# Performance work log

Measured on AMD Instinct MI355X. Metric: run time of the kernel, lower is better.

Reference implementation:

```python
import jax, jax.numpy as jnp
import numpy as np

D_EQUI, D_INV, D_MSG, N_HEADS, D_FF = 64, 256, 64, 8, 256
D_EDGE_IN, D_EDGE_OUT = 64, 64
D_OUT = D_EQUI + N_HEADS + D_EDGE_OUT  # 136
IN_FEATS = 2 * D_MSG + D_EQUI + D_EDGE_IN  # 256
B, N = 4, 256
NEG_INF = -1e9  # finite stand-in for -inf in adj_to_attn_mask


def setup_inputs() -> dict:
    key = jax.random.key(0)
    ks = jax.random.split(key, 20)
    def rn(k, shape, scale):
        return jax.random.normal(k, shape, dtype=jnp.float32) * scale
    inp = {
        "equis": rn(ks[0], (B, N, 3, D_EQUI), 1.0),
        "invs": rn(ks[1], (B, N, D_INV), 1.0),
        "edges": rn(ks[2], (B, N, N, D_EDGE_IN), 1.0),
        "adj_matrix": jax.random.randint(ks[3], (B, N, N), 0, 2, dtype=jnp.int32),
        # _PairwiseMessages params
        "Wq": rn(ks[4], (D_MSG, D_INV), D_INV ** -0.5),
        "bq": jnp.zeros((D_MSG,), jnp.float32),
        "Wk": rn(ks[5], (D_MSG, D_INV), D_INV ** -0.5),
        "bk": jnp.zeros((D_MSG,), jnp.float32),
        "W1": rn(ks[6], (D_FF, IN_FEATS), IN_FEATS ** -0.5),
        "b1": jnp.zeros((D_FF,), jnp.float32),
        "W2": rn(ks[7], (D_OUT, D_FF), D_FF ** -0.5),
        "b2": jnp.zeros((D_OUT,), jnp.float32),
        # _EquiAttention params (no bias)
        "Wc": rn(ks[8], (D_EQUI, D_EQUI), D_EQUI ** -0.5),
        "Wa": rn(ks[9], (D_EQUI, D_EQUI), D_EQUI ** -0.5),
        # _InvAttention params
        "Wi": rn(ks[10], (D_INV, D_INV), D_INV ** -0.5),
        "bi": jnp.zeros((D_INV,), jnp.float32),
        "Wo": rn(ks[11], (D_INV, D_INV), D_INV ** -0.5),
        "bo": jnp.zeros((D_INV,), jnp.float32),
    }
    return inp


def _forward(equis, invs, edges, adj_matrix, Wq, bq, Wk, bk, W1, b1, W2, b2, Wc, Wa, Wi, bi, Wo, bo):
    # ---- _PairwiseMessages ----
    # per-channel dot products over the 3 coordinates: [B, Nq, Nk, d_equi]
    dotprods = jnp.einsum("bqcd,bkcd->bqkd", equis, equis)
    q_msg = invs @ Wq.T + bq          # [B, N, d_msg]
    k_msg = invs @ Wk.T + bk          # [B, N, d_msg]
    Nq = invs.shape[1]
    pairwise = jnp.concatenate(
        (
            jnp.broadcast_to(q_msg[:, :, None, :], (B, Nq, Nq, D_MSG)),
            jnp.broadcast_to(k_msg[:, None, :, :], (B, Nq, Nq, D_MSG)),
            dotprods,
            edges,
        ),
        axis=-1,
    )  # [B, Nq, Nk, in_feats]
    h = jax.nn.silu(pairwise @ W1.T + b1)
    messages = h @ W2.T + b2          # [B, Nq, Nk, d_out]

    equi_msg = messages[..., :D_EQUI]
    inv_msg = messages[..., D_EQUI : D_EQUI + N_HEADS]
    edge_out = messages[..., D_EQUI + N_HEADS :]

    attn_mask = jnp.where(adj_matrix > 0, 0.0, NEG_INF).astype(equi_msg.dtype)  # [B,Nq,Nk]

    # ---- _EquiAttention ----
    attn_e = jax.nn.softmax(equi_msg + attn_mask[..., None], axis=2)  # [B,Nq,Nk,d_equi]
    proj_equi = equis @ Wc.T                                          # [B,Nk,3,d_equi]
    attn_out_e = jnp.einsum("bqkd,bkcd->bqcd", attn_e, proj_equi)     # [B,Nq,3,d_equi]
    w_e = jnp.sqrt(jnp.sum(attn_e ** 2, axis=2))                      # [B,Nq,d_equi]
    attn_out_e = attn_out_e * w_e[:, :, None, :]
    equi_updates = attn_out_e @ Wa.T

    # ---- _InvAttention ----
    attn_i = jax.nn.softmax(inv_msg + attn_mask[..., None], axis=2)   # [B,Nq,Nk,H]
    proj_feats = invs @ Wi.T + bi                                     # [B,Nk,d_inv]
    head_feats = proj_feats.reshape(B, Nq, N_HEADS, D_INV // N_HEADS)
    attn_out_i = jnp.einsum("bqkh,bkhd->bqhd", attn_i, head_feats)    # [B,Nq,H,d_head]
    w_i = jnp.sqrt(jnp.sum(attn_i ** 2, axis=2))                      # [B,Nq,H]
    attn_out_i = attn_out_i * w_i[..., None]
    inv_updates = attn_out_i.reshape(B, Nq, D_INV) @ Wo.T + bo

    return equi_updates, inv_updates, edge_out


def reference(equis, invs, edges, adj_matrix, Wq, bq, Wk, bk, W1, b1, W2, b2, Wc, Wa, Wi, bi, Wo, bo):
    return _forward(equis, invs, edges, adj_matrix, Wq, bq, Wk, bk, W1, b1, W2, b2, Wc, Wa, Wi, bi, Wo, bo)
```

## Files before the change

kernel.cpp:

```cpp
#include <hip/hip_runtime.h>
#include <hip/hip_bf16.h>
#include <cstdint>


typedef __bf16 bf16x4_t __attribute__((ext_vector_type(4)));
typedef __bf16 bf16x8_t __attribute__((ext_vector_type(8)));
typedef float  f32x4_t  __attribute__((ext_vector_type(4)));

#define SP 76
#define KV 32

__device__ __forceinline__ int swzX(int row, int col) {
    return row * 192 + (col ^ ((row & 7) << 3));
}
__device__ __forceinline__ int swzH(int row, int col) {
    return (row << 8) + (col ^ ((row & 7) << 3));
}

__device__ __forceinline__ bf16x8_t cvt8(f32x4_t a, f32x4_t b) {
    bf16x8_t r;
    r[0] = (__bf16)a.x; r[1] = (__bf16)a.y; r[2] = (__bf16)a.z; r[3] = (__bf16)a.w;
    r[4] = (__bf16)b.x; r[5] = (__bf16)b.y; r[6] = (__bf16)b.z; r[7] = (__bf16)b.w;
    return r;
}
__device__ __forceinline__ bf16x4_t cvt4(f32x4_t a) {
    bf16x4_t r;
    r[0] = (__bf16)a.x; r[1] = (__bf16)a.y; r[2] = (__bf16)a.z; r[3] = (__bf16)a.w;
    return r;
}

__global__ __launch_bounds__(256) void semla_pre(
    const float* __restrict__ invs, const float* __restrict__ equis,
    const float* __restrict__ Wq, const float* __restrict__ bq,
    const float* __restrict__ Wk, const float* __restrict__ bk,
    const float* __restrict__ Wc, const float* __restrict__ Wi, const float* __restrict__ bi,
    const float* __restrict__ W1, const float* __restrict__ W2,
    __bf16* __restrict__ W1bf, __bf16* __restrict__ W2bf,
    float* __restrict__ qc, float* __restrict__ kmsg,
    float* __restrict__ pTE, float* __restrict__ pTF)
{
    const int blk = blockIdx.x, tid = threadIdx.x;
    if (blk < 256) {
        const int r0 = blk * 4;
        __shared__ __align__(16) float sInv4[4][256];
        __shared__ __align__(16) float sEqu4[4][192];
        __shared__ __align__(16) float sQm4[4][64];
        #pragma unroll
        for (int j = 0; j < 4; ++j) {
            sInv4[j][tid] = invs[(size_t)(r0 + j) * 256 + tid];
            if (tid < 192) sEqu4[j][tid] = equis[(size_t)(r0 + j) * 192 + tid];
        }
        __syncthreads();
        {
            float acc[4] = {0.f, 0.f, 0.f, 0.f};
            const float* w = &Wi[tid * 256];
            for (int i = 0; i < 256; i += 4) {
                f32x4_t ww = *(const f32x4_t*)&w[i];
                #pragma unroll
                for (int j = 0; j < 4; ++j) {
                    const float* x = &sInv4[j][i];
                    acc[j] += ww.x * x[0] + ww.y * x[1] + ww.z * x[2] + ww.w * x[3];
                }
            }
            const float bb = bi[tid];
            #pragma unroll
            for (int j = 0; j < 4; ++j) {
                const int bb_ = (r0 + j) >> 8, nl = (r0 + j) & 255;
                pTF[((size_t)bb_ * 256 + tid) * 256 + nl] = acc[j] + bb;
            }
        }
        if (tid < 128) {
            const int d = tid & 63;
            const float* w = (tid < 64) ? &Wq[d * 256] : &Wk[d * 256];
            float acc[4] = {0.f, 0.f, 0.f, 0.f};
            for (int i = 0; i < 256; i += 4) {
                f32x4_t ww = *(const f32x4_t*)&w[i];
                #pragma unroll
                for (int j = 0; j < 4; ++j) {
                    const float* x = &sInv4[j][i];
                    acc[j] += ww.x * x[0] + ww.y * x[1] + ww.z * x[2] + ww.w * x[3];
                }
            }
            if (tid < 64) {
                const float bb = bq[d];
                #pragma unroll
                for (int j = 0; j < 4; ++j) sQm4[j][d] = acc[j] + bb;
            } else {
                const float bb = bk[d];
                #pragma unroll
                for (int j = 0; j < 4; ++j) kmsg[(size_t)(r0 + j) * 64 + d] = acc[j] + bb;
            }
        }
        if (tid < 192) {
            const int c = tid >> 6, e = tid & 63;
            const float* w = &Wc[e * 64];
            float acc[4] = {0.f, 0.f, 0.f, 0.f};
            for (int dd = 0; dd < 64; dd += 4) {
                f32x4_t ww = *(const f32x4_t*)&w[dd];
                #pragma unroll
                for (int j = 0; j < 4; ++j) {
                    const float* x = &sEqu4[j][c * 64 + dd];
                    acc[j] += ww.x * x[0] + ww.y * x[1] + ww.z * x[2] + ww.w * x[3];
                }
            }
            #pragma unroll
            for (int j = 0; j < 4; ++j) {
                const int bb_ = (r0 + j) >> 8, nl = (r0 + j) & 255;
                pTE[(((size_t)bb_ * 3 + c) * 64 + e) * 256 + nl] = acc[j];
            }
        }
        __syncthreads();
        {
            const float* w = &W1[tid * 256];
            float acc[4] = {0.f, 0.f, 0.f, 0.f};
            for (int d = 0; d < 64; d += 4) {
                f32x4_t ww = *(const f32x4_t*)&w[d];
                #pragma unroll
                for (int j = 0; j < 4; ++j) {
                    const float* x = &sQm4[j][d];
                    acc[j] += ww.x * x[0] + ww.y * x[1] + ww.z * x[2] + ww.w * x[3];
                }
            }
            #pragma unroll
            for (int j = 0; j < 4; ++j) qc[(size_t)(r0 + j) * 256 + tid] = acc[j];
        }
    } else if (blk < 268) {
        const int base = (blk - 256) * 4096;
        #pragma unroll
        for (int it = 0; it < 16; ++it) {
            const int e = base + it * 256 + tid;
            const int o = e / 192, k = e % 192;
            W1bf[e] = (__bf16)W1[o * 256 + 64 + k];
        }
    } else if (blk < 277) {
        const int base = (blk - 268) * 4096;
        #pragma unroll
        for (int it = 0; it < 16; ++it) {
            const int e = base + it * 256 + tid;
            const int o = e >> 8, cc = e & 255;
            const int src = (o < 64) ? (72 + o) : (o < 136 ? o - 64 : -1);
            W2bf[e] = (src >= 0) ? (__bf16)W2[src * 256 + cc] : (__bf16)0.f;
        }
    }
}

__global__ __launch_bounds__(512, 2) void semla_main(
    const float* __restrict__ equis, const float* __restrict__ edges,
    const int* __restrict__ adj,
    const __bf16* __restrict__ W1bf, const __bf16* __restrict__ W2bf,
    const float* __restrict__ qc, const float* __restrict__ kmsg,
    const float* __restrict__ pTE, const float* __restrict__ pTF,
    const float* __restrict__ b1, const float* __restrict__ b2,
    float* __restrict__ outE, float* __restrict__ outI, float* __restrict__ outEdge)
{
    const int bqid = ((blockIdx.x & 7) << 7) | (blockIdx.x >> 3);
    const int b = bqid >> 8;
    const int tid = threadIdx.x;
    const int wave = tid >> 6, lane = tid & 63;
    const int arow = lane & 15, kgrp = lane >> 4;

    __shared__ __align__(16) __bf16 sX[KV * 192];
    __shared__ __align__(16) __bf16 sH[KV * 256];
    __shared__ __align__(16) float  sS[KV * SP];
    __shared__ __align__(16) float  sB1[256];
    __shared__ __align__(16) float  sB2[144];
    __shared__ __align__(16) float  sEquiQ[192];
    __shared__ float sF[72], sL[72], sL2[72];
    __shared__ int   sAdj[2][KV];

    if (tid < 256) sB1[tid] = b1[tid] + qc[(size_t)bqid * 256 + tid];
    if (tid < 144) sB2[tid] = (tid < 64) ? b2[72 + tid] : (tid < 136 ? b2[tid - 64] : 0.f);
    if (tid < 192) sEquiQ[tid] = equis[(size_t)bqid * 192 + tid];

    bf16x8_t w1r[6][2];
    #pragma unroll
    for (int ks = 0; ks < 6; ++ks)
        #pragma unroll
        for (int cf = 0; cf < 2; ++cf)
            w1r[ks][cf] = *(const bf16x8_t*)
                &W1bf[((wave << 5) + (cf << 4) + arow) * 192 + ks * 32 + (kgrp << 3)];
    bf16x8_t w2r[8], w2r2[8];
    #pragma unroll
    for (int ks = 0; ks < 8; ++ks)
        w2r[ks] = *(const bf16x8_t*)
            &W2bf[(((wave << 4) + arow) << 8) + ks * 32 + (kgrp << 3)];
    if (wave == 7) {
        #pragma unroll
        for (int ks = 0; ks < 8; ++ks)
            w2r2[ks] = *(const bf16x8_t*)
                &W2bf[((128 + arow) << 8) + ks * 32 + (kgrp << 3)];
    }

    float m_run = -1e30f, l_run = 0.f, l2_run = 0.f;
    float m_rn2 = -1e30f, l_rn2 = 0.f, l2_rn2 = 0.f;
    float accE = 0.f;
    float accI = 0.f;
    const int c_e = tid >> 6, d_e = tid & 63;
    const int fidx = tid - 256, h_i = (tid - 256) >> 5;

    const int rowS = (tid & 255) >> 3;
    const int c8S = (tid & 7) << 3;
    const int pchunk = tid >> 1, prow = pchunk >> 3;
    const int pcol = 128 + ((pchunk & 7) << 3) + ((tid & 1) << 2);

    __syncthreads();

    {
        if (tid < 256) {
            const float* p = &kmsg[(size_t)(b * 256 + rowS) * 64 + c8S];
            *(bf16x8_t*)&sX[swzX(rowS, c8S)] =
                cvt8(*(const f32x4_t*)p, *(const f32x4_t*)(p + 4));
        } else {
            const float* ek = &equis[(size_t)(b * 256 + rowS) * 192 + c8S];
            f32x4_t e0a = *(const f32x4_t*)(ek),       e0b = *(const f32x4_t*)(ek + 4);
            f32x4_t e1a = *(const f32x4_t*)(ek + 64),  e1b = *(const f32x4_t*)(ek + 68);
            f32x4_t e2a = *(const f32x4_t*)(ek + 128), e2b = *(const f32x4_t*)(ek + 132);
            f32x4_t q0a = *(const f32x4_t*)&sEquiQ[c8S],       q0b = *(const f32x4_t*)&sEquiQ[c8S + 4];
            f32x4_t q1a = *(const f32x4_t*)&sEquiQ[64 + c8S],  q1b = *(const f32x4_t*)&sEquiQ[68 + c8S];
            f32x4_t q2a = *(const f32x4_t*)&sEquiQ[128 + c8S], q2b = *(const f32x4_t*)&sEquiQ[132 + c8S];
            *(bf16x8_t*)&sX[swzX(rowS, 64 + c8S)] =
                cvt8(e0a * q0a + e1a * q1a + e2a * q2a,
                     e0b * q0b + e1b * q1b + e2b * q2b);
        }
        f32x4_t ed = *(const f32x4_t*)&edges[((size_t)bqid * 256 + prow) * 64 + (pcol - 128)];
        *(bf16x4_t*)&sX[swzX(prow, pcol)] = cvt4(ed);
        if (tid < KV) sAdj[0][tid] = adj[(size_t)bqid * 256 + tid];
    }
    __syncthreads();

    for (int kt = 0; kt < 8; ++kt) {
        const int k0 = kt * KV;
        const int cur = kt & 1;

        f32x4_t edPf = {0.f, 0.f, 0.f, 0.f};
        if (kt < 7)
            edPf = *(const f32x4_t*)
                &edges[((size_t)bqid * 256 + k0 + KV + prow) * 64 + (pcol - 128)];

        if (kt > 0) {
            const int k0P = k0 - KV;
            if (tid < 192) {
                float a = accE * sF[d_e];
                const float* pe = &pTE[(((size_t)b * 3 + c_e) * 64 + d_e) * 256 + k0P];
                #pragma unroll
                for (int t = 0; t < 8; ++t) {
                    f32x4_t w = *(const f32x4_t*)&pe[t * 4];
                    a += sS[(4 * t + 0) * SP + d_e] * w.x;
                    a += sS[(4 * t + 1) * SP + d_e] * w.y;
                    a += sS[(4 * t + 2) * SP + d_e] * w.z;
                    a += sS[(4 * t + 3) * SP + d_e] * w.w;
                }
                accE = a;
            }
            if (tid >= 256) {
                float a = accI * sF[64 + h_i];
                const float* pf = &pTF[((size_t)b * 256 + fidx) * 256 + k0P];
                #pragma unroll
                for (int t = 0; t < 8; ++t) {
                    f32x4_t w = *(const f32x4_t*)&pf[t * 4];
                    a += sS[(4 * t + 0) * SP + 64 + h_i] * w.x;
                    a += sS[(4 * t + 1) * SP + 64 + h_i] * w.y;
                    a += sS[(4 * t + 2) * SP + 64 + h_i] * w.z;
                    a += sS[(4 * t + 3) * SP + 64 + h_i] * w.w;
                }
                accI = a;
            }
        }

        f32x4_t acc1[2][2];
        {
            const f32x4_t z = {0.f, 0.f, 0.f, 0.f};
            acc1[0][0] = z; acc1[0][1] = z; acc1[1][0] = z; acc1[1][1] = z;
        }
        #pragma unroll
        for (int ks = 0; ks < 6; ++ks) {
            const int kk = ks * 32 + (kgrp << 3);
            bf16x8_t a0 = *(const bf16x8_t*)&sX[swzX(arow, kk)];
            bf16x8_t a1 = *(const bf16x8_t*)&sX[swzX(16 + arow, kk)];
            acc1[0][0] = __builtin_amdgcn_mfma_f32_16x16x32_bf16(a0, w1r[ks][0], acc1[0][0], 0, 0, 0);
            acc1[0][1] = __builtin_amdgcn_mfma_f32_16x16x32_bf16(a0, w1r[ks][1], acc1[0][1], 0, 0, 0);
            acc1[1][0] = __builtin_amdgcn_mfma_f32_16x16x32_bf16(a1, w1r[ks][0], acc1[1][0], 0, 0, 0);
            acc1[1][1] = __builtin_amdgcn_mfma_f32_16x16x32_bf16(a1, w1r[ks][1], acc1[1][1], 0, 0, 0);
        }
        #pragma unroll
        for (int rt = 0; rt < 2; ++rt)
            #pragma unroll
            for (int cf = 0; cf < 2; ++cf) {
                const int ccol = (wave << 5) + (cf << 4) + arow;
                const float bb = sB1[ccol];
                #pragma unroll
                for (int j = 0; j < 4; ++j) {
                    const int row = (rt << 4) + (kgrp << 2) + j;
                    float x = acc1[rt][cf][j] + bb;
                    sH[swzH(row, ccol)] = (__bf16)(x / (1.f + __expf(-x)));
                }
            }
        __syncthreads();

        f32x4_t kmA, kmB;
        f32x4_t e0a_, e0b_, e1a_, e1b_, e2a_, e2b_;
        int adjN = 0;
        if (kt < 7) {
            const int kbN = b * 256 + k0 + KV;
            if (tid < 256) {
                const float* p = &kmsg[(size_t)(kbN + rowS) * 64 + c8S];
                kmA = *(const f32x4_t*)p;
                kmB = *(const f32x4_t*)(p + 4);
            } else {
                const float* ek = &equis[(size_t)(kbN + rowS) * 192 + c8S];
                e0a_ = *(const f32x4_t*)(ek);       e0b_ = *(const f32x4_t*)(ek + 4);
                e1a_ = *(const f32x4_t*)(ek + 64);  e1b_ = *(const f32x4_t*)(ek + 68);
                e2a_ = *(const f32x4_t*)(ek + 128); e2b_ = *(const f32x4_t*)(ek + 132);
            }
            if (tid < KV) adjN = adj[(size_t)bqid * 256 + k0 + KV + tid];
        }

        f32x4_t acc2[2], acc2b[2];
        {
            const f32x4_t z = {0.f, 0.f, 0.f, 0.f};
            acc2[0] = z; acc2[1] = z; acc2b[0] = z; acc2b[1] = z;
        }
        #pragma unroll
        for (int ks = 0; ks < 8; ++ks) {
            const int kk = ks * 32 + (kgrp << 3);
            bf16x8_t a0 = *(const bf16x8_t*)&sH[swzH(arow, kk)];
            bf16x8_t a1 = *(const bf16x8_t*)&sH[swzH(16 + arow, kk)];
            acc2[0] = __builtin_amdgcn_mfma_f32_16x16x32_bf16(a0, w2r[ks], acc2[0], 0, 0, 0);
            acc2[1] = __builtin_amdgcn_mfma_f32_16x16x32_bf16(a1, w2r[ks], acc2[1], 0, 0, 0);
            if (wave == 7) {
                acc2b[0] = __builtin_amdgcn_mfma_f32_16x16x32_bf16(a0, w2r2[ks], acc2b[0], 0, 0, 0);
                acc2b[1] = __builtin_amdgcn_mfma_f32_16x16x32_bf16(a1, w2r2[ks], acc2b[1], 0, 0, 0);
            }
        }
        const int col = (wave << 4) + arow;
        if (wave < 4) {
            const float bb2 = sB2[col];
            #pragma unroll
            for (int rt = 0; rt < 2; ++rt)
                #pragma unroll
                for (int j = 0; j < 4; ++j) {
                    const int r = (rt << 4) + (kgrp << 2) + j;
                    outEdge[((size_t)bqid * 256 + k0 + r) * 64 + col] = acc2[rt][j] + bb2;
                }
        } else {
            const int ch = col - 64;
            const float bb2 = sB2[col];
            float s_[8]; int ad_[8];
            float xm = -1e30f;
            #pragma unroll
            for (int rt = 0; rt < 2; ++rt)
                #pragma unroll
                for (int j = 0; j < 4; ++j) {
                    const int r = (rt << 4) + (kgrp << 2) + j;
                    const float v = acc2[rt][j] + bb2;
                    s_[rt * 4 + j] = v;
                    ad_[rt * 4 + j] = sAdj[cur][r];
                    if (ad_[rt * 4 + j]) xm = fmaxf(xm, v);
                }
            xm = fmaxf(xm, __shfl_xor(xm, 16));
            xm = fmaxf(xm, __shfl_xor(xm, 32));
            const float mN = fmaxf(m_run, xm);
            const float f = __expf(m_run - mN);
            float s1 = 0.f, s2 = 0.f;
            #pragma unroll
            for (int rt = 0; rt < 2; ++rt)
                #pragma unroll
                for (int j = 0; j < 4; ++j) {
                    const int r = (rt << 4) + (kgrp << 2) + j;
                    const float p = ad_[rt * 4 + j] ? __expf(s_[rt * 4 + j] - mN) : 0.f;
                    sS[r * SP + ch] = p;
                    s1 += p; s2 += p * p;
                }
            s1 += __shfl_xor(s1, 16); s1 += __shfl_xor(s1, 32);
            s2 += __shfl_xor(s2, 16); s2 += __shfl_xor(s2, 32);
            l_run = l_run * f + s1;
            l2_run = l2_run * f * f + s2;
            m_run = mN;
            if (kgrp == 0) sF[ch] = f;
        }
        if (wave == 7) {
            const float bb3 = sB2[128 + (arow & 7)];
            float s_[8]; int ad_[8];
            float xm = -1e30f;
            #pragma unroll
            for (int rt = 0; rt < 2; ++rt)
                #pragma unroll
                for (int j = 0; j < 4; ++j) {
                    const int r = (rt << 4) + (kgrp << 2) + j;
                    const float v = acc2b[rt][j] + bb3;
                    s_[rt * 4 + j] = v;
                    ad_[rt * 4 + j] = sAdj[cur][r];
                    if (ad_[rt * 4 + j]) xm = fmaxf(xm, v);
                }
            xm = fmaxf(xm, __shfl_xor(xm, 16));
            xm = fmaxf(xm, __shfl_xor(xm, 32));
            const float mN = fmaxf(m_rn2, xm);
            const float f = __expf(m_rn2 - mN);
            float s1 = 0.f, s2 = 0.f;
            #pragma unroll
            for (int rt = 0; rt < 2; ++rt)
                #pragma unroll
                for (int j = 0; j < 4; ++j) {
                    const int r = (rt << 4) + (kgrp << 2) + j;
                    const float p = ad_[rt * 4 + j] ? __expf(s_[rt * 4 + j] - mN) : 0.f;
                    if (arow < 8) sS[r * SP + 64 + arow] = p;
                    s1 += p; s2 += p * p;
                }
            s1 += __shfl_xor(s1, 16); s1 += __shfl_xor(s1, 32);
            s2 += __shfl_xor(s2, 16); s2 += __shfl_xor(s2, 32);
            l_rn2 = l_rn2 * f + s1;
            l2_rn2 = l2_rn2 * f * f + s2;
            m_rn2 = mN;
            if (kgrp == 0 && arow < 8) sF[64 + arow] = f;
        }

        if (kt < 7) {
            if (tid < 256) {
                *(bf16x8_t*)&sX[swzX(rowS, c8S)] = cvt8(kmA, kmB);
            } else {
                f32x4_t q0a = *(const f32x4_t*)&sEquiQ[c8S],       q0b = *(const f32x4_t*)&sEquiQ[c8S + 4];
                f32x4_t q1a = *(const f32x4_t*)&sEquiQ[64 + c8S],  q1b = *(const f32x4_t*)&sEquiQ[68 + c8S];
                f32x4_t q2a = *(const f32x4_t*)&sEquiQ[128 + c8S], q2b = *(const f32x4_t*)&sEquiQ[132 + c8S];
                *(bf16x8_t*)&sX[swzX(rowS, 64 + c8S)] =
                    cvt8(e0a_ * q0a + e1a_ * q1a + e2a_ * q2a,
                         e0b_ * q0b + e1b_ * q1b + e2b_ * q2b);
            }
            *(bf16x4_t*)&sX[swzX(prow, pcol)] = cvt4(edPf);
            if (tid < KV) sAdj[cur ^ 1][tid] = adjN;
        }
        __syncthreads();
    }

    {
        const int k0P = 224;
        if (tid < 192) {
            float a = accE * sF[d_e];
            const float* pe = &pTE[(((size_t)b * 3 + c_e) * 64 + d_e) * 256 + k0P];
            #pragma unroll
            for (int t = 0; t < 8; ++t) {
                f32x4_t w = *(const f32x4_t*)&pe[t * 4];
                a += sS[(4 * t + 0) * SP + d_e] * w.x;
                a += sS[(4 * t + 1) * SP + d_e] * w.y;
                a += sS[(4 * t + 2) * SP + d_e] * w.z;
                a += sS[(4 * t + 3) * SP + d_e] * w.w;
            }
            accE = a;
        }
        if (tid >= 256) {
            float a = accI * sF[64 + h_i];
            const float* pf = &pTF[((size_t)b * 256 + fidx) * 256 + k0P];
            #pragma unroll
            for (int t = 0; t < 8; ++t) {
                f32x4_t w = *(const f32x4_t*)&pf[t * 4];
                a += sS[(4 * t + 0) * SP + 64 + h_i] * w.x;
                a += sS[(4 * t + 1) * SP + 64 + h_i] * w.y;
                a += sS[(4 * t + 2) * SP + 64 + h_i] * w.z;
                a += sS[(4 * t + 3) * SP + 64 + h_i] * w.w;
            }
            accI = a;
        }
    }

    if (wave >= 4 && kgrp == 0) {
        const int ch = ((wave - 4) << 4) + arow;
        sL[ch] = l_run; sL2[ch] = l2_run;
        if (wave == 7 && arow < 8) { sL[64 + arow] = l_rn2; sL2[64 + arow] = l2_rn2; }
    }
    __syncthreads();
    if (tid < 192) {
        const float ll = sL[d_e];
        outE[(size_t)bqid * 192 + tid] = accE * sqrtf(sL2[d_e]) / (ll * ll);
    }
    if (tid >= 256) {
        const float ll = sL[64 + h_i];
        outI[(size_t)bqid * 256 + fidx] = accI * sqrtf(sL2[64 + h_i]) / (ll * ll);
    }
}

__global__ __launch_bounds__(256) void semla_post(
    const float* __restrict__ Wa, const float* __restrict__ Wo,
    const float* __restrict__ bo,
    float* __restrict__ outE, float* __restrict__ outI)
{
    __shared__ __align__(16) float hE[4][192];
    __shared__ __align__(16) float hI[4][256];
    const int blk = blockIdx.x, tid = threadIdx.x;
    const int r0 = blk * 4;
    #pragma unroll
    for (int r = 0; r < 4; ++r) {
        if (tid < 192) hE[r][tid] = outE[(size_t)(r0 + r) * 192 + tid];
        hI[r][tid] = outI[(size_t)(r0 + r) * 256 + tid];
    }
    __syncthreads();
    if (tid < 192) {
        const int c = tid >> 6, e = tid & 63;
        float wa[64];
        #pragma unroll
        for (int d = 0; d < 64; d += 4) {
            f32x4_t w = *(const f32x4_t*)&Wa[e * 64 + d];
            wa[d] = w.x; wa[d + 1] = w.y; wa[d + 2] = w.z; wa[d + 3] = w.w;
        }
        #pragma unroll
        for (int r = 0; r < 4; ++r) {
            float s = 0.f;
            #pragma unroll
            for (int d = 0; d < 64; ++d) s += hE[r][c * 64 + d] * wa[d];
            outE[((size_t)(r0 + r) * 3 + c) * 64 + e] = s;
        }
    }
    {
        const float bb = bo[tid];
        const float* wo = &Wo[tid * 256];
        #pragma unroll
        for (int r = 0; r < 4; ++r) {
            float s = 0.f;
            for (int i = 0; i < 256; i += 4) {
                f32x4_t w = *(const f32x4_t*)&wo[i];
                s += w.x * hI[r][i] + w.y * hI[r][i + 1]
                   + w.z * hI[r][i + 2] + w.w * hI[r][i + 3];
            }
            outI[(size_t)(r0 + r) * 256 + tid] = s + bb;
        }
    }
}

extern "C" void kernel_launch(void* const* d_in, const int* in_sizes, int n_in,
                              void* d_out, int out_size, void* d_ws, size_t ws_size,
                              hipStream_t stream) {
    (void)in_sizes; (void)n_in; (void)out_size; (void)ws_size;
    const float* equis = (const float*)d_in[0];
    const float* invs  = (const float*)d_in[1];
    const float* edges = (const float*)d_in[2];
    const int*   adj   = (const int*)d_in[3];
    const float* Wq = (const float*)d_in[4];
    const float* bq = (const float*)d_in[5];
    const float* Wk = (const float*)d_in[6];
    const float* bk = (const float*)d_in[7];
    const float* W1 = (const float*)d_in[8];
    const float* b1 = (const float*)d_in[9];
    const float* W2 = (const float*)d_in[10];
    const float* b2 = (const float*)d_in[11];
    const float* Wc = (const float*)d_in[12];
    const float* Wa = (const float*)d_in[13];
    const float* Wi = (const float*)d_in[14];
    const float* bi = (const float*)d_in[15];
    const float* Wo = (const float*)d_in[16];
    const float* bo = (const float*)d_in[17];

    float* out = (float*)d_out;
    float* outE    = out;
    float* outI    = out + 196608;
    float* outEdge = out + 458752;

    char* ws = (char*)d_ws;
    __bf16* W1bf = (__bf16*)(ws);
    __bf16* W2bf = (__bf16*)(ws + 98304);
    float* qc    = (float*)(ws + 172032);
    float* kmsg  = (float*)(ws + 1220608);
    float* pTE   = (float*)(ws + 1482752);
    float* pTF   = (float*)(ws + 2269184);

    semla_pre<<<277, 256, 0, stream>>>(invs, equis, Wq, bq, Wk, bk, Wc, Wi, bi,
                                       W1, W2, W1bf, W2bf, qc, kmsg, pTE, pTF);
    semla_main<<<1024, 512, 0, stream>>>(equis, edges, adj, W1bf, W2bf, qc, kmsg,
                                         pTE, pTF, b1, b2,
                                         outE, outI, outEdge);
    semla_post<<<256, 256, 0, stream>>>(Wa, Wo, bo, outE, outI);
}
```

Before: 299.0 us.

## Double main kernel block to 1024 threads, splitting MFMA tiles across 16 waves

New measurement: 338.4 us. 1.13x slower.

```diff
diff --git a/kernel.cpp b/kernel.cpp
--- a/kernel.cpp
+++ b/kernel.cpp
@@ -144,7 +144,7 @@
     }
 }
 
-__global__ __launch_bounds__(512, 2) void semla_main(
+__global__ __launch_bounds__(1024, 4) void semla_main(
     const float* __restrict__ equis, const float* __restrict__ edges,
     const int* __restrict__ adj,
     const __bf16* __restrict__ W1bf, const __bf16* __restrict__ W2bf,
@@ -172,58 +172,54 @@
     if (tid < 144) sB2[tid] = (tid < 64) ? b2[72 + tid] : (tid < 136 ? b2[tid - 64] : 0.f);
     if (tid < 192) sEquiQ[tid] = equis[(size_t)bqid * 192 + tid];
 
-    bf16x8_t w1r[6][2];
+    bf16x8_t w1r[6];
     #pragma unroll
     for (int ks = 0; ks < 6; ++ks)
-        #pragma unroll
-        for (int cf = 0; cf < 2; ++cf)
-            w1r[ks][cf] = *(const bf16x8_t*)
-                &W1bf[((wave << 5) + (cf << 4) + arow) * 192 + ks * 32 + (kgrp << 3)];
-    bf16x8_t w2r[8], w2r2[8];
+        w1r[ks] = *(const bf16x8_t*)
+            &W1bf[((wave << 4) + arow) * 192 + ks * 32 + (kgrp << 3)];
+    const int w2row = (((wave <= 8) ? wave : 0) << 4) + arow;
+    bf16x8_t w2r[8];
     #pragma unroll
     for (int ks = 0; ks < 8; ++ks)
-        w2r[ks] = *(const bf16x8_t*)
-            &W2bf[(((wave << 4) + arow) << 8) + ks * 32 + (kgrp << 3)];
-    if (wave == 7) {
-        #pragma unroll
-        for (int ks = 0; ks < 8; ++ks)
-            w2r2[ks] = *(const bf16x8_t*)
-                &W2bf[((128 + arow) << 8) + ks * 32 + (kgrp << 3)];
-    }
+        w2r[ks] = *(const bf16x8_t*)&W2bf[(w2row << 8) + ks * 32 + (kgrp << 3)];
 
     float m_run = -1e30f, l_run = 0.f, l2_run = 0.f;
-    float m_rn2 = -1e30f, l_rn2 = 0.f, l2_rn2 = 0.f;
     float accE = 0.f;
     float accI = 0.f;
     const int c_e = tid >> 6, d_e = tid & 63;
     const int fidx = tid - 256, h_i = (tid - 256) >> 5;
-
-    const int rowS = (tid & 255) >> 3;
-    const int c8S = (tid & 7) << 3;
-    const int pchunk = tid >> 1, prow = pchunk >> 3;
-    const int pcol = 128 + ((pchunk & 7) << 3) + ((tid & 1) << 2);
+    const bool isE = (tid < 192), isI = (tid >= 256 && tid < 512);
+    const bool sm = (wave >= 4 && wave <= 8);
+    const bool chOK = (wave < 8) || (arow < 8);
+    const int ch = ((wave - 4) << 4) + arow;
+
+    const int rowK = tid >> 3,          c8K = (tid & 7) << 3;
+    const int rowD = (tid - 256) >> 3,  c8D = ((tid - 256) & 7) << 3;
+    const int rowE = (tid - 512) >> 4,  c4E = (((tid - 512) & 15) << 2) + 128;
 
     __syncthreads();
 
     {
         if (tid < 256) {
-            const float* p = &kmsg[(size_t)(b * 256 + rowS) * 64 + c8S];
-            *(bf16x8_t*)&sX[swzX(rowS, c8S)] =
+            const float* p = &kmsg[(size_t)(b * 256 + rowK) * 64 + c8K];
+            *(bf16x8_t*)&sX[swzX(rowK, c8K)] =
                 cvt8(*(const f32x4_t*)p, *(const f32x4_t*)(p + 4));
-        } else {
-            const float* ek = &equis[(size_t)(b * 256 + rowS) * 192 + c8S];
+        } else if (tid < 512) {
+            const float* ek = &equis[(size_t)(b * 256 + rowD) * 192 + c8D];
             f32x4_t e0a = *(const f32x4_t*)(ek),       e0b = *(const f32x4_t*)(ek + 4);
             f32x4_t e1a = *(const f32x4_t*)(ek + 64),  e1b = *(const f32x4_t*)(ek + 68);
             f32x4_t e2a = *(const f32x4_t*)(ek + 128), e2b = *(const f32x4_t*)(ek + 132);
-            f32x4_t q0a = *(const f32x4_t*)&sEquiQ[c8S],       q0b = *(const f32x4_t*)&sEquiQ[c8S + 4];
-            f32x4_t q1a = *(const f32x4_t*)&sEquiQ[64 + c8S],  q1b = *(const f32x4_t*)&sEquiQ[68 + c8S];
-            f32x4_t q2a = *(const f32x4_t*)&sEquiQ[128 + c8S], q2b = *(const f32x4_t*)&sEquiQ[132 + c8S];
-            *(bf16x8_t*)&sX[swzX(rowS, 64 + c8S)] =
+            f32x4_t q0a = *(const f32x4_t*)&sEquiQ[c8D],       q0b = *(const f32x4_t*)&sEquiQ[c8D + 4];
+            f32x4_t q1a = *(const f32x4_t*)&sEquiQ[64 + c8D],  q1b = *(const f32x4_t*)&sEquiQ[68 + c8D];
+            f32x4_t q2a = *(const f32x4_t*)&sEquiQ[128 + c8D], q2b = *(const f32x4_t*)&sEquiQ[132 + c8D];
+            *(bf16x8_t*)&sX[swzX(rowD, 64 + c8D)] =
                 cvt8(e0a * q0a + e1a * q1a + e2a * q2a,
                      e0b * q0b + e1b * q1b + e2b * q2b);
-        }
-        f32x4_t ed = *(const f32x4_t*)&edges[((size_t)bqid * 256 + prow) * 64 + (pcol - 128)];
-        *(bf16x4_t*)&sX[swzX(prow, pcol)] = cvt4(ed);
+        } else {
+            f32x4_t ed = *(const f32x4_t*)
+                &edges[((size_t)bqid * 256 + rowE) * 64 + (c4E - 128)];
+            *(bf16x4_t*)&sX[swzX(rowE, c4E)] = cvt4(ed);
+        }
         if (tid < KV) sAdj[0][tid] = adj[(size_t)bqid * 256 + tid];
     }
     __syncthreads();
@@ -233,13 +229,13 @@
         const int cur = kt & 1;
 
         f32x4_t edPf = {0.f, 0.f, 0.f, 0.f};
-        if (kt < 7)
+        if (kt < 7 && tid >= 512)
             edPf = *(const f32x4_t*)
-                &edges[((size_t)bqid * 256 + k0 + KV + prow) * 64 + (pcol - 128)];
+                &edges[((size_t)bqid * 256 + k0 + KV + rowE) * 64 + (c4E - 128)];
 
         if (kt > 0) {
             const int k0P = k0 - KV;
-            if (tid < 192) {
+            if (isE) {
                 float a = accE * sF[d_e];
                 const float* pe = &pTE[(((size_t)b * 3 + c_e) * 64 + d_e) * 256 + k0P];
                 #pragma unroll
@@ -252,7 +248,7 @@
                 }
                 accE = a;
             }
-            if (tid >= 256) {
+            if (isI) {
                 float a = accI * sF[64 + h_i];
                 const float* pf = &pTF[((size_t)b * 256 + fidx) * 256 + k0P];
                 #pragma unroll
@@ -267,34 +263,31 @@
             }
         }
 
-        f32x4_t acc1[2][2];
+        f32x4_t acc1[2];
         {
             const f32x4_t z = {0.f, 0.f, 0.f, 0.f};
-            acc1[0][0] = z; acc1[0][1] = z; acc1[1][0] = z; acc1[1][1] = z;
+            acc1[0] = z; acc1[1] = z;
         }
         #pragma unroll
         for (int ks = 0; ks < 6; ++ks) {
             const int kk = ks * 32 + (kgrp << 3);
             bf16x8_t a0 = *(const bf16x8_t*)&sX[swzX(arow, kk)];
             bf16x8_t a1 = *(const bf16x8_t*)&sX[swzX(16 + arow, kk)];
-            acc1[0][0] = __builtin_amdgcn_mfma_f32_16x16x32_bf16(a0, w1r[ks][0], acc1[0][0], 0, 0, 0);
-            acc1[0][1] = __builtin_amdgcn_mfma_f32_16x16x32_bf16(a0, w1r[ks][1], acc1[0][1], 0, 0, 0);
-            acc1[1][0] = __builtin_amdgcn_mfma_f32_16x16x32_bf16(a1, w1r[ks][0], acc1[1][0], 0, 0, 0);
-            acc1[1][1] = __builtin_amdgcn_mfma_f32_16x16x32_bf16(a1, w1r[ks][1], acc1[1][1], 0, 0, 0);
-        }
-        #pragma unroll
-        for (int rt = 0; rt < 2; ++rt)
-            #pragma unroll
-            for (int cf = 0; cf < 2; ++cf) {
-                const int ccol = (wave << 5) + (cf << 4) + arow;
-                const float bb = sB1[ccol];
+            acc1[0] = __builtin_amdgcn_mfma_f32_16x16x32_bf16(a0, w1r[ks], acc1[0], 0, 0, 0);
+            acc1[1] = __builtin_amdgcn_mfma_f32_16x16x32_bf16(a1, w1r[ks], acc1[1], 0, 0, 0);
+        }
+        {
+            const int ccol = (wave << 4) + arow;
+            const float bb = sB1[ccol];
+            #pragma unroll
+            for (int rt = 0; rt < 2; ++rt)
                 #pragma unroll
                 for (int j = 0; j < 4; ++j) {
                     const int row = (rt << 4) + (kgrp << 2) + j;
-                    float x = acc1[rt][cf][j] + bb;
+                    float x = acc1[rt][j] + bb;
                     sH[swzH(row, ccol)] = (__bf16)(x / (1.f + __expf(-x)));
                 }
-            }
+        }
         __syncthreads();
 
         f32x4_t kmA, kmB;
@@ -303,11 +296,11 @@
         if (kt < 7) {
             const int kbN = b * 256 + k0 + KV;
             if (tid < 256) {
-                const float* p = &kmsg[(size_t)(kbN + rowS) * 64 + c8S];
+                const float* p = &kmsg[(size_t)(kbN + rowK) * 64 + c8K];
                 kmA = *(const f32x4_t*)p;
                 kmB = *(const f32x4_t*)(p + 4);
-            } else {
-                const float* ek = &equis[(size_t)(kbN + rowS) * 192 + c8S];
+            } else if (tid < 512) {
+                const float* ek = &equis[(size_t)(kbN + rowD) * 192 + c8D];
                 e0a_ = *(const f32x4_t*)(ek);       e0b_ = *(const f32x4_t*)(ek + 4);
                 e1a_ = *(const f32x4_t*)(ek + 64);  e1b_ = *(const f32x4_t*)(ek + 68);
                 e2a_ = *(const f32x4_t*)(ek + 128); e2b_ = *(const f32x4_t*)(ek + 132);
@@ -315,117 +308,84 @@
             if (tid < KV) adjN = adj[(size_t)bqid * 256 + k0 + KV + tid];
         }
 
-        f32x4_t acc2[2], acc2b[2];
-        {
-            const f32x4_t z = {0.f, 0.f, 0.f, 0.f};
-            acc2[0] = z; acc2[1] = z; acc2b[0] = z; acc2b[1] = z;
-        }
-        #pragma unroll
-        for (int ks = 0; ks < 8; ++ks) {
-            const int kk = ks * 32 + (kgrp << 3);
-            bf16x8_t a0 = *(const bf16x8_t*)&sH[swzH(arow, kk)];
-            bf16x8_t a1 = *(const bf16x8_t*)&sH[swzH(16 + arow, kk)];
-            acc2[0] = __builtin_amdgcn_mfma_f32_16x16x32_bf16(a0, w2r[ks], acc2[0], 0, 0, 0);
-            acc2[1] = __builtin_amdgcn_mfma_f32_16x16x32_bf16(a1, w2r[ks], acc2[1], 0, 0, 0);
-            if (wave == 7) {
-                acc2b[0] = __builtin_amdgcn_mfma_f32_16x16x32_bf16(a0, w2r2[ks], acc2b[0], 0, 0, 0);
-                acc2b[1] = __builtin_amdgcn_mfma_f32_16x16x32_bf16(a1, w2r2[ks], acc2b[1], 0, 0, 0);
-            }
-        }
-        const int col = (wave << 4) + arow;
-        if (wave < 4) {
-            const float bb2 = sB2[col];
-            #pragma unroll
-            for (int rt = 0; rt < 2; ++rt)
-                #pragma unroll
-                for (int j = 0; j < 4; ++j) {
-                    const int r = (rt << 4) + (kgrp << 2) + j;
-                    outEdge[((size_t)bqid * 256 + k0 + r) * 64 + col] = acc2[rt][j] + bb2;
-                }
-        } else {
-            const int ch = col - 64;
-            const float bb2 = sB2[col];
-            float s_[8]; int ad_[8];
-            float xm = -1e30f;
-            #pragma unroll
-            for (int rt = 0; rt < 2; ++rt)
-                #pragma unroll
-                for (int j = 0; j < 4; ++j) {
-                    const int r = (rt << 4) + (kgrp << 2) + j;
-                    const float v = acc2[rt][j] + bb2;
-                    s_[rt * 4 + j] = v;
-                    ad_[rt * 4 + j] = sAdj[cur][r];
-                    if (ad_[rt * 4 + j]) xm = fmaxf(xm, v);
-                }
-            xm = fmaxf(xm, __shfl_xor(xm, 16));
-            xm = fmaxf(xm, __shfl_xor(xm, 32));
-            const float mN = fmaxf(m_run, xm);
-            const float f = __expf(m_run - mN);
-            float s1 = 0.f, s2 = 0.f;
-            #pragma unroll
-            for (int rt = 0; rt < 2; ++rt)
-                #pragma unroll
-                for (int j = 0; j < 4; ++j) {
-                    const int r = (rt << 4) + (kgrp << 2) + j;
-                    const float p = ad_[rt * 4 + j] ? __expf(s_[rt * 4 + j] - mN) : 0.f;
-                    sS[r * SP + ch] = p;
-                    s1 += p; s2 += p * p;
-                }
-            s1 += __shfl_xor(s1, 16); s1 += __shfl_xor(s1, 32);
-            s2 += __shfl_xor(s2, 16); s2 += __shfl_xor(s2, 32);
-            l_run = l_run * f + s1;
-            l2_run = l2_run * f * f + s2;
-            m_run = mN;
-            if (kgrp == 0) sF[ch] = f;
-        }
-        if (wave == 7) {
-            const float bb3 = sB2[128 + (arow & 7)];
-            float s_[8]; int ad_[8];
-            float xm = -1e30f;
-            #pragma unroll
-            for (int rt = 0; rt < 2; ++rt)
-                #pragma unroll
-                for (int j = 0; j < 4; ++j) {
-                    const int r = (rt << 4) + (kgrp << 2) + j;
-                    const float v = acc2b[rt][j] + bb3;
-                    s_[rt * 4 + j] = v;
-                    ad_[rt * 4 + j] = sAdj[cur][r];
-                    if (ad_[rt * 4 + j]) xm = fmaxf(xm, v);
-                }
-            xm = fmaxf(xm, __shfl_xor(xm, 16));
-            xm = fmaxf(xm, __shfl_xor(xm, 32));
-            const float mN = fmaxf(m_rn2, xm);
-            const float f = __expf(m_rn2 - mN);
-            float s1 = 0.f, s2 = 0.f;
-            #pragma unroll
-            for (int rt = 0; rt < 2; ++rt)
-                #pragma unroll
-                for (int j = 0; j < 4; ++j) {
-                    const int r = (rt << 4) + (kgrp << 2) + j;
-                    const float p = ad_[rt * 4 + j] ? __expf(s_[rt * 4 + j] - mN) : 0.f;
-                    if (arow < 8) sS[r * SP + 64 + arow] = p;
-                    s1 += p; s2 += p * p;
-                }
-            s1 += __shfl_xor(s1, 16); s1 += __shfl_xor(s1, 32);
-            s2 += __shfl_xor(s2, 16); s2 += __shfl_xor(s2, 32);
-            l_rn2 = l_rn2 * f + s1;
-            l2_rn2 = l2_rn2 * f * f + s2;
-            m_rn2 = mN;
-            if (kgrp == 0 && arow < 8) sF[64 + arow] = f;
+        if (wave <= 8) {
+            f32x4_t acc2[2];
+            {
+                const f32x4_t z = {0.f, 0.f, 0.f, 0.f};
+                acc2[0] = z; acc2[1] = z;
+            }
+            #pragma unroll
+            for (int ks = 0; ks < 8; ++ks) {
+                const int kk = ks * 32 + (kgrp << 3);
+                bf16x8_t a0 = *(const bf16x8_t*)&sH[swzH(arow, kk)];
+                bf16x8_t a1 = *(const bf16x8_t*)&sH[swzH(16 + arow, kk)];
+                acc2[0] = __builtin_amdgcn_mfma_f32_16x16x32_bf16(a0, w2r[ks], acc2[0], 0, 0, 0);
+                acc2[1] = __builtin_amdgcn_mfma_f32_16x16x32_bf16(a1, w2r[ks], acc2[1], 0, 0, 0);
+            }
+            if (wave < 4) {
+                const int col = (wave << 4) + arow;
+                const float bb2 = sB2[col];
+                #pragma unroll
+                for (int rt = 0; rt < 2; ++rt)
+                    #pragma unroll
+                    for (int j = 0; j < 4; ++j) {
+                        const int r = (rt << 4) + (kgrp << 2) + j;
+                        outEdge[((size_t)bqid * 256 + k0 + r) * 64 + col] = acc2[rt][j] + bb2;
+                    }
+            } else {
+                const float bb2 = sB2[(wave << 4) + arow];
+                float s_[8];
+                unsigned adm = 0;
+                float xm = -1e30f;
+                #pragma unroll
+                for (int rt = 0; rt < 2; ++rt)
+                    #pragma unroll
+                    for (int j = 0; j < 4; ++j) {
+                        const int r = (rt << 4) + (kgrp << 2) + j;
+                        const float v = acc2[rt][j] + bb2;
+                        s_[rt * 4 + j] = v;
+                        if (sAdj[cur][r]) {
+                            adm |= (1u << (rt * 4 + j));
+                            xm = fmaxf(xm, v);
+                        }
+                    }
+                xm = fmaxf(xm, __shfl_xor(xm, 16));
+                xm = fmaxf(xm, __shfl_xor(xm, 32));
+                const float mN = fmaxf(m_run, xm);
+                const float f = __expf(m_run - mN);
+                float s1 = 0.f, s2 = 0.f;
+                #pragma unroll
+                for (int rt = 0; rt < 2; ++rt)
+                    #pragma unroll
+                    for (int j = 0; j < 4; ++j) {
+                        const int r = (rt << 4) + (kgrp << 2) + j;
+                        const float p = ((adm >> (rt * 4 + j)) & 1u)
+                                        ? __expf(s_[rt * 4 + j] - mN) : 0.f;
+                        if (chOK) sS[r * SP + ch] = p;
+                        s1 += p; s2 += p * p;
+                    }
+                s1 += __shfl_xor(s1, 16); s1 += __shfl_xor(s1, 32);
+                s2 += __shfl_xor(s2, 16); s2 += __shfl_xor(s2, 32);
+                l_run = l_run * f + s1;
+                l2_run = l2_run * f * f + s2;
+                m_run = mN;
+                if (kgrp == 0 && chOK) sF[ch] = f;
+            }
         }
 
         if (kt < 7) {
             if (tid < 256) {
-                *(bf16x8_t*)&sX[swzX(rowS, c8S)] = cvt8(kmA, kmB);
-            } else {
-                f32x4_t q0a = *(const f32x4_t*)&sEquiQ[c8S],       q0b = *(const f32x4_t*)&sEquiQ[c8S + 4];
-                f32x4_t q1a = *(const f32x4_t*)&sEquiQ[64 + c8S],  q1b = *(const f32x4_t*)&sEquiQ[68 + c8S];
-                f32x4_t q2a = *(const f32x4_t*)&sEquiQ[128 + c8S], q2b = *(const f32x4_t*)&sEquiQ[132 + c8S];
-                *(bf16x8_t*)&sX[swzX(rowS, 64 + c8S)] =
+                *(bf16x8_t*)&sX[swzX(rowK, c8K)] = cvt8(kmA, kmB);
+            } else if (tid < 512) {
+                f32x4_t q0a = *(const f32x4_t*)&sEquiQ[c8D],       q0b = *(const f32x4_t*)&sEquiQ[c8D + 4];
+                f32x4_t q1a = *(const f32x4_t*)&sEquiQ[64 + c8D],  q1b = *(const f32x4_t*)&sEquiQ[68 + c8D];
+                f32x4_t q2a = *(const f32x4_t*)&sEquiQ[128 + c8D], q2b = *(const f32x4_t*)&sEquiQ[132 + c8D];
+                *(bf16x8_t*)&sX[swzX(rowD, 64 + c8D)] =
                     cvt8(e0a_ * q0a + e1a_ * q1a + e2a_ * q2a,
                          e0b_ * q0b + e1b_ * q1b + e2b_ * q2b);
-            }
-            *(bf16x4_t*)&sX[swzX(prow, pcol)] = cvt4(edPf);
+            } else {
+                *(bf16x4_t*)&sX[swzX(rowE, c4E)] = cvt4(edPf);
+            }
             if (tid < KV) sAdj[cur ^ 1][tid] = adjN;
         }
         __syncthreads();
@@ -433,7 +393,7 @@
 
     {
         const int k0P = 224;
-        if (tid < 192) {
+        if (isE) {
             float a = accE * sF[d_e];
             const float* pe = &pTE[(((size_t)b * 3 + c_e) * 64 + d_e) * 256 + k0P];
             #pragma unroll
@@ -446,7 +406,7 @@
             }
             accE = a;
         }
-        if (tid >= 256) {
+        if (isI) {
             float a = accI * sF[64 + h_i];
             const float* pf = &pTF[((size_t)b * 256 + fidx) * 256 + k0P];
             #pragma unroll
@@ -461,17 +421,13 @@
         }
     }
 
-    if (wave >= 4 && kgrp == 0) {
-        const int ch = ((wave - 4) << 4) + arow;
-        sL[ch] = l_run; sL2[ch] = l2_run;
-        if (wave == 7 && arow < 8) { sL[64 + arow] = l_rn2; sL2[64 + arow] = l2_rn2; }
-    }
+    if (sm && kgrp == 0 && chOK) { sL[ch] = l_run; sL2[ch] = l2_run; }
     __syncthreads();
-    if (tid < 192) {
+    if (isE) {
         const float ll = sL[d_e];
         outE[(size_t)bqid * 192 + tid] = accE * sqrtf(sL2[d_e]) / (ll * ll);
     }
-    if (tid >= 256) {
+    if (isI) {
         const float ll = sL[64 + h_i];
         outI[(size_t)bqid * 256 + fidx] = accI * sqrtf(sL2[64 + h_i]) / (ll * ll);
     }
@@ -562,8 +518,8 @@
 
     semla_pre<<<277, 256, 0, stream>>>(invs, equis, Wq, bq, Wk, bk, Wc, Wi, bi,
                                        W1, W2, W1bf, W2bf, qc, kmsg, pTE, pTF);
-    semla_main<<<1024, 512, 0, stream>>>(equis, edges, adj, W1bf, W2bf, qc, kmsg,
-                                         pTE, pTF, b1, b2,
-                                         outE, outI, outEdge);
+    semla_main<<<1024, 1024, 0, stream>>>(equis, edges, adj, W1bf, W2bf, qc, kmsg,
+                                          pTE, pTF, b1, b2,
+                                          outE, outI, outEdge);
     semla_post<<<256, 256, 0, stream>>>(Wa, Wo, bo, outE, outI);
 }
```
